# Optimization experiments

Hardware: AMD Instinct MI355X
Metric: run time of the kernel (lower is better)

Reference implementation:

```python
import jax, jax.numpy as jnp
import numpy as np

INPUT_CH = 32
INPUT_CH_VIEWS = 16
HIDDEN = 64
GEO_FEAT = 15
N_PTS = 2097152


def _kaiming(key, in_dim, out_dim):
    # mimic nn.Linear default init (kaiming uniform, fan_in)
    bound = 1.0 / np.sqrt(in_dim)
    return jax.random.uniform(key, (in_dim, out_dim), jnp.float32, -bound, bound)


def setup_inputs() -> dict:
    key = jax.random.key(0)
    ks = jax.random.split(key, 8)
    x = jax.random.normal(ks[0], (N_PTS, INPUT_CH + INPUT_CH_VIEWS), jnp.float32)
    # sigma net: 32 -> 64 -> 64 -> 16 (1 sigma + 15 geo feat), bias-free
    s0 = _kaiming(ks[1], INPUT_CH, HIDDEN)
    s1 = _kaiming(ks[2], HIDDEN, HIDDEN)
    s2 = _kaiming(ks[3], HIDDEN, 1 + GEO_FEAT)
    # color net: (16 views + 15 geo) = 31 -> 64 -> 64 -> 3, bias-free
    c0 = _kaiming(ks[4], INPUT_CH_VIEWS + GEO_FEAT, HIDDEN)
    c1 = _kaiming(ks[5], HIDDEN, HIDDEN)
    c2 = _kaiming(ks[6], HIDDEN, HIDDEN)
    c3 = _kaiming(ks[7], HIDDEN, 3)
    return {"x": x, "s0": s0, "s1": s1, "s2": s2,
            "c0": c0, "c1": c1, "c2": c2, "c3": c3}


def reference(x, s0, s1, s2, c0, c1, c2, c3):
    input_pts = x[..., :INPUT_CH]
    input_views = x[..., INPUT_CH:]
    # sigma net: ReLU between layers, no activation on last
    h = jax.nn.relu(input_pts @ s0)
    h = jax.nn.relu(h @ s1)
    h = h @ s2                      # [N, 1 + geo_feat]
    sigma = h[..., 0]
    geo_feat = h[..., 1:]
    # color net
    h = jnp.concatenate([input_views, geo_feat], axis=-1)
    h = jax.nn.relu(h @ c0)
    h = jax.nn.relu(h @ c1)
    h = jax.nn.relu(h @ c2)
    color = h @ c3                  # [N, 3]
    return jnp.concatenate([color, sigma[..., None]], axis=-1)  # [N, 4]
```

## Files before the change

### kernel.cpp

```cpp
#include <hip/hip_runtime.h>


typedef _Float16 half8  __attribute__((ext_vector_type(8)));
typedef _Float16 half4v __attribute__((ext_vector_type(4)));
typedef float    floatx4 __attribute__((ext_vector_type(4)));

#define NPTS   2097152
#define NTILES (NPTS / 64)
#define XS     72

__device__ __forceinline__ half8 load_bfrag(const float* __restrict__ W,
                                            int Kr, int Nr, int n, int kbase) {
    half8 f;
#pragma unroll
    for (int j = 0; j < 8; ++j) {
        int k = kbase + j;
        float v = (k < Kr && n < Nr) ? W[k * Nr + n] : 0.0f;
        f[j] = (_Float16)v;
    }
    return f;
}

__global__ __launch_bounds__(256, 2)
void nerf_fused(const float* __restrict__ x,
                const float* __restrict__ ws0, const float* __restrict__ ws1,
                const float* __restrict__ ws2, const float* __restrict__ wc0,
                const float* __restrict__ wc1, const float* __restrict__ wc2,
                const float* __restrict__ wc3, float* __restrict__ out) {
    __shared__ __align__(16) _Float16 sX[4][16][XS];
    __shared__ __align__(16) _Float16 sH[4][16][XS];
    __shared__ __align__(16) float    sO[4][16][4];

    const int tid  = threadIdx.x;
    const int w    = tid >> 6;
    const int lane = tid & 63;
    const int l16  = lane & 15;
    const int quad = lane >> 4;

    half8 Bs0[4], Bc0[4], Bs2[2], Bc3[2];
    half8 Bs1[4][2], Bc1[4][2], Bc2[4][2];
#pragma unroll
    for (int nt = 0; nt < 4; ++nt) {
        Bs0[nt] = load_bfrag(ws0, 32, 64, nt*16 + l16, quad*8);
        Bc0[nt] = load_bfrag(wc0, 31, 64, nt*16 + l16, quad*8);
#pragma unroll
        for (int ks = 0; ks < 2; ++ks) {
            Bs1[nt][ks] = load_bfrag(ws1, 64, 64, nt*16 + l16, ks*32 + quad*8);
            Bc1[nt][ks] = load_bfrag(wc1, 64, 64, nt*16 + l16, ks*32 + quad*8);
            Bc2[nt][ks] = load_bfrag(wc2, 64, 64, nt*16 + l16, ks*32 + quad*8);
        }
    }
#pragma unroll
    for (int ks = 0; ks < 2; ++ks) {
        Bs2[ks] = load_bfrag(ws2, 64, 16, l16, ks*32 + quad*8);
        Bc3[ks] = load_bfrag(wc3, 64,  3, l16, ks*32 + quad*8);
    }

    if (lane < 16) sX[w][lane][63] = (_Float16)0.0f;

    const floatx4 vzero = {0.f, 0.f, 0.f, 0.f};

    int srow[3], scol[3];
#pragma unroll
    for (int p = 0; p < 3; ++p) {
        int t = lane + 64*p;
        srow[p] = t / 12;
        scol[p] = (t % 12) * 4;
    }

    int tile = blockIdx.x;
    float4 xv0, xv1, xv2;
    {
        const float4* xb = (const float4*)(x + (size_t)(tile*64 + w*16) * 48);
        xv0 = xb[lane]; xv1 = xb[lane + 64]; xv2 = xb[lane + 128];
    }

    while (tile < NTILES) {
        int next = tile + gridDim.x;
        int pf = next < NTILES ? next : tile;
        const float4* xb = (const float4*)(x + (size_t)(pf*64 + w*16) * 48);
        float4 nv0 = xb[lane], nv1 = xb[lane + 64], nv2 = xb[lane + 128];

        float4 vv[3] = {xv0, xv1, xv2};
#pragma unroll
        for (int p = 0; p < 3; ++p) {
            half4v h;
            h[0] = (_Float16)vv[p].x; h[1] = (_Float16)vv[p].y;
            h[2] = (_Float16)vv[p].z; h[3] = (_Float16)vv[p].w;
            *(half4v*)&sX[w][srow[p]][scol[p]] = h;
        }

        floatx4 acc[4];

        half8 a0 = *(const half8*)&sX[w][l16][quad*8];
#pragma unroll
        for (int nt = 0; nt < 4; ++nt)
            acc[nt] = __builtin_amdgcn_mfma_f32_16x16x32_f16(a0, Bs0[nt], vzero, 0, 0, 0);
#pragma unroll
        for (int nt = 0; nt < 4; ++nt)
#pragma unroll
            for (int i = 0; i < 4; ++i)
                sH[w][quad*4 + i][nt*16 + l16] = (_Float16)fmaxf(acc[nt][i], 0.f);

        half8 a1 = *(const half8*)&sH[w][l16][quad*8];
        half8 a2 = *(const half8*)&sH[w][l16][32 + quad*8];
#pragma unroll
        for (int nt = 0; nt < 4; ++nt) {
            acc[nt] = __builtin_amdgcn_mfma_f32_16x16x32_f16(a1, Bs1[nt][0], vzero,  0, 0, 0);
            acc[nt] = __builtin_amdgcn_mfma_f32_16x16x32_f16(a2, Bs1[nt][1], acc[nt], 0, 0, 0);
        }
#pragma unroll
        for (int nt = 0; nt < 4; ++nt)
#pragma unroll
            for (int i = 0; i < 4; ++i)
                sH[w][quad*4 + i][nt*16 + l16] = (_Float16)fmaxf(acc[nt][i], 0.f);

        a1 = *(const half8*)&sH[w][l16][quad*8];
        a2 = *(const half8*)&sH[w][l16][32 + quad*8];
        floatx4 accS = __builtin_amdgcn_mfma_f32_16x16x32_f16(a1, Bs2[0], vzero, 0, 0, 0);
        accS         = __builtin_amdgcn_mfma_f32_16x16x32_f16(a2, Bs2[1], accS,  0, 0, 0);
#pragma unroll
        for (int i = 0; i < 4; ++i) {
            int row = quad*4 + i;
            if (l16 == 0) sO[w][row][3] = accS[i];
            else          sX[w][row][47 + l16] = (_Float16)accS[i];
        }

        half8 a3 = *(const half8*)&sX[w][l16][32 + quad*8];
#pragma unroll
        for (int nt = 0; nt < 4; ++nt)
            acc[nt] = __builtin_amdgcn_mfma_f32_16x16x32_f16(a3, Bc0[nt], vzero, 0, 0, 0);
#pragma unroll
        for (int nt = 0; nt < 4; ++nt)
#pragma unroll
            for (int i = 0; i < 4; ++i)
                sH[w][quad*4 + i][nt*16 + l16] = (_Float16)fmaxf(acc[nt][i], 0.f);

        a1 = *(const half8*)&sH[w][l16][quad*8];
        a2 = *(const half8*)&sH[w][l16][32 + quad*8];
#pragma unroll
        for (int nt = 0; nt < 4; ++nt) {
            acc[nt] = __builtin_amdgcn_mfma_f32_16x16x32_f16(a1, Bc1[nt][0], vzero,  0, 0, 0);
            acc[nt] = __builtin_amdgcn_mfma_f32_16x16x32_f16(a2, Bc1[nt][1], acc[nt], 0, 0, 0);
        }
#pragma unroll
        for (int nt = 0; nt < 4; ++nt)
#pragma unroll
            for (int i = 0; i < 4; ++i)
                sH[w][quad*4 + i][nt*16 + l16] = (_Float16)fmaxf(acc[nt][i], 0.f);

        a1 = *(const half8*)&sH[w][l16][quad*8];
        a2 = *(const half8*)&sH[w][l16][32 + quad*8];
#pragma unroll
        for (int nt = 0; nt < 4; ++nt) {
            acc[nt] = __builtin_amdgcn_mfma_f32_16x16x32_f16(a1, Bc2[nt][0], vzero,  0, 0, 0);
            acc[nt] = __builtin_amdgcn_mfma_f32_16x16x32_f16(a2, Bc2[nt][1], acc[nt], 0, 0, 0);
        }
#pragma unroll
        for (int nt = 0; nt < 4; ++nt)
#pragma unroll
            for (int i = 0; i < 4; ++i)
                sH[w][quad*4 + i][nt*16 + l16] = (_Float16)fmaxf(acc[nt][i], 0.f);

        a1 = *(const half8*)&sH[w][l16][quad*8];
        a2 = *(const half8*)&sH[w][l16][32 + quad*8];
        floatx4 accC = __builtin_amdgcn_mfma_f32_16x16x32_f16(a1, Bc3[0], vzero, 0, 0, 0);
        accC         = __builtin_amdgcn_mfma_f32_16x16x32_f16(a2, Bc3[1], accC,  0, 0, 0);
        if (l16 < 3) {
#pragma unroll
            for (int i = 0; i < 4; ++i)
                sO[w][quad*4 + i][l16] = accC[i];
        }

        if (lane < 16) {
            float4 o = *(const float4*)&sO[w][lane][0];
            ((float4*)out)[(size_t)tile*64 + w*16 + lane] = o;
        }

        xv0 = nv0; xv1 = nv1; xv2 = nv2;
        tile = next;
    }
}

extern "C" void kernel_launch(void* const* d_in, const int* in_sizes, int n_in,
                              void* d_out, int out_size, void* d_ws, size_t ws_size,
                              hipStream_t stream) {
    nerf_fused<<<1024, 256, 0, stream>>>(
        (const float*)d_in[0], (const float*)d_in[1], (const float*)d_in[2],
        (const float*)d_in[3], (const float*)d_in[4], (const float*)d_in[5],
        (const float*)d_in[6], (const float*)d_in[7], (float*)d_out);
}
```

Baseline: 656.3 us.

## Transpose MLP to keep activations in registers and prepack fp16 weights

The per-wave MLP is reformulated as W^T·X^T, so the MFMA output layout of one layer feeds the next layer's B operand directly. This removes the shared-memory round trips between layers, and the weight K-dimension is permuted to match. A small pre-kernel packs all weights into fp16 fragment order in the workspace, so the main kernel does one coalesced load per fragment instead of scattered fp32 gathers. Input rows are loaded directly in fragment layout, and sigma and color are written straight from the accumulators. The cost is an extra kernel launch per call and a fragile index permutation that must stay consistent.

Measured after the change: 549.3 us. 1.19x faster.

```diff
diff --git a/kernel.cpp b/kernel.cpp
--- a/kernel.cpp
+++ b/kernel.cpp
@@ -2,182 +2,150 @@
 
 
 typedef _Float16 half8  __attribute__((ext_vector_type(8)));
-typedef _Float16 half4v __attribute__((ext_vector_type(4)));
 typedef float    floatx4 __attribute__((ext_vector_type(4)));
 
 #define NPTS   2097152
 #define NTILES (NPTS / 64)
-#define XS     72
 
-__device__ __forceinline__ half8 load_bfrag(const float* __restrict__ W,
-                                            int Kr, int Nr, int n, int kbase) {
-    half8 f;
+__global__ void prep_weights(const float* __restrict__ ws0, const float* __restrict__ ws1,
+                             const float* __restrict__ ws2, const float* __restrict__ wc0,
+                             const float* __restrict__ wc1, const float* __restrict__ wc2,
+                             const float* __restrict__ wc3, _Float16* __restrict__ wpack) {
+    int t = blockIdx.x * blockDim.x + threadIdx.x;
+    if (t >= 36 * 64) return;
+    int fid = t >> 6, lane = t & 63, l16 = lane & 15, q = lane >> 4;
 #pragma unroll
     for (int j = 0; j < 8; ++j) {
-        int k = kbase + j;
-        float v = (k < Kr && n < Nr) ? W[k * Nr + n] : 0.0f;
-        f[j] = (_Float16)v;
+        int phi = (2 * 0 + (j >> 2)) * 16 + q * 4 + (j & 3);
+        float v = 0.f;
+        if (fid < 4) {
+            v = ws0[(q * 8 + j) * 64 + fid * 16 + l16];
+        } else if (fid < 12) {
+            int mt = (fid - 4) >> 1, c = (fid - 4) & 1;
+            int p = (2 * c + (j >> 2)) * 16 + q * 4 + (j & 3);
+            v = ws1[p * 64 + mt * 16 + l16];
+        } else if (fid < 14) {
+            int c = fid - 12;
+            int p = (2 * c + (j >> 2)) * 16 + q * 4 + (j & 3);
+            v = ws2[p * 16 + l16];
+        } else if (fid < 18) {
+            int mt = fid - 14;
+            if (j < 4) v = wc0[(q * 4 + j) * 64 + mt * 16 + l16];
+            else {
+                int g = q * 4 + (j - 4);
+                v = (g == 0) ? 0.f : wc0[(15 + g) * 64 + mt * 16 + l16];
+            }
+        } else if (fid < 26) {
+            int mt = (fid - 18) >> 1, c = (fid - 18) & 1;
+            int p = (2 * c + (j >> 2)) * 16 + q * 4 + (j & 3);
+            v = wc1[p * 64 + mt * 16 + l16];
+        } else if (fid < 34) {
+            int mt = (fid - 26) >> 1, c = (fid - 26) & 1;
+            int p = (2 * c + (j >> 2)) * 16 + q * 4 + (j & 3);
+            v = wc2[p * 64 + mt * 16 + l16];
+        } else {
+            int c = fid - 34;
+            int p = (2 * c + (j >> 2)) * 16 + q * 4 + (j & 3);
+            v = (l16 < 3) ? wc3[p * 3 + l16] : 0.f;
+        }
+        (void)phi;
+        wpack[t * 8 + j] = (_Float16)v;
     }
-    return f;
+}
+
+__device__ __forceinline__ half8 packrelu(floatx4 a, floatx4 b) {
+    half8 r;
+    r[0] = (_Float16)fmaxf(a[0], 0.f); r[1] = (_Float16)fmaxf(a[1], 0.f);
+    r[2] = (_Float16)fmaxf(a[2], 0.f); r[3] = (_Float16)fmaxf(a[3], 0.f);
+    r[4] = (_Float16)fmaxf(b[0], 0.f); r[5] = (_Float16)fmaxf(b[1], 0.f);
+    r[6] = (_Float16)fmaxf(b[2], 0.f); r[7] = (_Float16)fmaxf(b[3], 0.f);
+    return r;
 }
 
 __global__ __launch_bounds__(256, 2)
-void nerf_fused(const float* __restrict__ x,
-                const float* __restrict__ ws0, const float* __restrict__ ws1,
-                const float* __restrict__ ws2, const float* __restrict__ wc0,
-                const float* __restrict__ wc1, const float* __restrict__ wc2,
-                const float* __restrict__ wc3, float* __restrict__ out) {
-    __shared__ __align__(16) _Float16 sX[4][16][XS];
-    __shared__ __align__(16) _Float16 sH[4][16][XS];
-    __shared__ __align__(16) float    sO[4][16][4];
+void nerf_fused(const float* __restrict__ x, const _Float16* __restrict__ wpack,
+                float* __restrict__ out) {
+    const int lane = threadIdx.x & 63;
+    const int w    = threadIdx.x >> 6;
+    const int l16  = lane & 15;
+    const int q    = lane >> 4;
 
-    const int tid  = threadIdx.x;
-    const int w    = tid >> 6;
-    const int lane = tid & 63;
-    const int l16  = lane & 15;
-    const int quad = lane >> 4;
+    half8 W[36];
+    const half8* wp = (const half8*)wpack;
+#pragma unroll
+    for (int f = 0; f < 36; ++f) W[f] = wp[f * 64 + lane];
 
-    half8 Bs0[4], Bc0[4], Bs2[2], Bc3[2];
-    half8 Bs1[4][2], Bc1[4][2], Bc2[4][2];
-#pragma unroll
-    for (int nt = 0; nt < 4; ++nt) {
-        Bs0[nt] = load_bfrag(ws0, 32, 64, nt*16 + l16, quad*8);
-        Bc0[nt] = load_bfrag(wc0, 31, 64, nt*16 + l16, quad*8);
-#pragma unroll
-        for (int ks = 0; ks < 2; ++ks) {
-            Bs1[nt][ks] = load_bfrag(ws1, 64, 64, nt*16 + l16, ks*32 + quad*8);
-            Bc1[nt][ks] = load_bfrag(wc1, 64, 64, nt*16 + l16, ks*32 + quad*8);
-            Bc2[nt][ks] = load_bfrag(wc2, 64, 64, nt*16 + l16, ks*32 + quad*8);
-        }
-    }
-#pragma unroll
-    for (int ks = 0; ks < 2; ++ks) {
-        Bs2[ks] = load_bfrag(ws2, 64, 16, l16, ks*32 + quad*8);
-        Bc3[ks] = load_bfrag(wc3, 64,  3, l16, ks*32 + quad*8);
-    }
-
-    if (lane < 16) sX[w][lane][63] = (_Float16)0.0f;
-
-    const floatx4 vzero = {0.f, 0.f, 0.f, 0.f};
-
-    int srow[3], scol[3];
-#pragma unroll
-    for (int p = 0; p < 3; ++p) {
-        int t = lane + 64*p;
-        srow[p] = t / 12;
-        scol[p] = (t % 12) * 4;
-    }
+    const floatx4 vz = {0.f, 0.f, 0.f, 0.f};
+    const float4* xb = (const float4*)x;
 
     int tile = blockIdx.x;
-    float4 xv0, xv1, xv2;
+    float4 vA, vB, vC;
     {
-        const float4* xb = (const float4*)(x + (size_t)(tile*64 + w*16) * 48);
-        xv0 = xb[lane]; xv1 = xb[lane + 64]; xv2 = xb[lane + 128];
+        size_t base = (size_t)(tile * 64 + w * 16 + l16) * 12;
+        vA = xb[base + q * 2]; vB = xb[base + q * 2 + 1]; vC = xb[base + 8 + q];
     }
 
     while (tile < NTILES) {
         int next = tile + gridDim.x;
         int pf = next < NTILES ? next : tile;
-        const float4* xb = (const float4*)(x + (size_t)(pf*64 + w*16) * 48);
-        float4 nv0 = xb[lane], nv1 = xb[lane + 64], nv2 = xb[lane + 128];
+        size_t nbase = (size_t)(pf * 64 + w * 16 + l16) * 12;
+        float4 nA = xb[nbase + q * 2], nB = xb[nbase + q * 2 + 1], nC = xb[nbase + 8 + q];
 
-        float4 vv[3] = {xv0, xv1, xv2};
+        half8 b0, b1;
+        b0[0] = (_Float16)vA.x; b0[1] = (_Float16)vA.y; b0[2] = (_Float16)vA.z; b0[3] = (_Float16)vA.w;
+        b0[4] = (_Float16)vB.x; b0[5] = (_Float16)vB.y; b0[6] = (_Float16)vB.z; b0[7] = (_Float16)vB.w;
+        floatx4 acc[4], a2[4];
 #pragma unroll
-        for (int p = 0; p < 3; ++p) {
-            half4v h;
-            h[0] = (_Float16)vv[p].x; h[1] = (_Float16)vv[p].y;
-            h[2] = (_Float16)vv[p].z; h[3] = (_Float16)vv[p].w;
-            *(half4v*)&sX[w][srow[p]][scol[p]] = h;
+        for (int mt = 0; mt < 4; ++mt)
+            acc[mt] = __builtin_amdgcn_mfma_f32_16x16x32_f16(W[mt], b0, vz, 0, 0, 0);
+
+        b0 = packrelu(acc[0], acc[1]); b1 = packrelu(acc[2], acc[3]);
+#pragma unroll
+        for (int mt = 0; mt < 4; ++mt) {
+            a2[mt] = __builtin_amdgcn_mfma_f32_16x16x32_f16(W[4 + mt * 2], b0, vz,     0, 0, 0);
+            a2[mt] = __builtin_amdgcn_mfma_f32_16x16x32_f16(W[5 + mt * 2], b1, a2[mt], 0, 0, 0);
         }
 
-        floatx4 acc[4];
+        b0 = packrelu(a2[0], a2[1]); b1 = packrelu(a2[2], a2[3]);
+        floatx4 accS;
+        accS = __builtin_amdgcn_mfma_f32_16x16x32_f16(W[12], b0, vz,   0, 0, 0);
+        accS = __builtin_amdgcn_mfma_f32_16x16x32_f16(W[13], b1, accS, 0, 0, 0);
+        float sigma = accS[0];
 
-        half8 a0 = *(const half8*)&sX[w][l16][quad*8];
+        half8 bc;
+        bc[0] = (_Float16)vC.x; bc[1] = (_Float16)vC.y; bc[2] = (_Float16)vC.z; bc[3] = (_Float16)vC.w;
+        bc[4] = (q == 0) ? (_Float16)0.f : (_Float16)accS[0];
+        bc[5] = (_Float16)accS[1]; bc[6] = (_Float16)accS[2]; bc[7] = (_Float16)accS[3];
 #pragma unroll
-        for (int nt = 0; nt < 4; ++nt)
-            acc[nt] = __builtin_amdgcn_mfma_f32_16x16x32_f16(a0, Bs0[nt], vzero, 0, 0, 0);
+        for (int mt = 0; mt < 4; ++mt)
+            acc[mt] = __builtin_amdgcn_mfma_f32_16x16x32_f16(W[14 + mt], bc, vz, 0, 0, 0);
+
+        b0 = packrelu(acc[0], acc[1]); b1 = packrelu(acc[2], acc[3]);
 #pragma unroll
-        for (int nt = 0; nt < 4; ++nt)
-#pragma unroll
-            for (int i = 0; i < 4; ++i)
-                sH[w][quad*4 + i][nt*16 + l16] = (_Float16)fmaxf(acc[nt][i], 0.f);
-
-        half8 a1 = *(const half8*)&sH[w][l16][quad*8];
-        half8 a2 = *(const half8*)&sH[w][l16][32 + quad*8];
-#pragma unroll
-        for (int nt = 0; nt < 4; ++nt) {
-            acc[nt] = __builtin_amdgcn_mfma_f32_16x16x32_f16(a1, Bs1[nt][0], vzero,  0, 0, 0);
-            acc[nt] = __builtin_amdgcn_mfma_f32_16x16x32_f16(a2, Bs1[nt][1], acc[nt], 0, 0, 0);
-        }
-#pragma unroll
-        for (int nt = 0; nt < 4; ++nt)
-#pragma unroll
-            for (int i = 0; i < 4; ++i)
-                sH[w][quad*4 + i][nt*16 + l16] = (_Float16)fmaxf(acc[nt][i], 0.f);
-
-        a1 = *(const half8*)&sH[w][l16][quad*8];
-        a2 = *(const half8*)&sH[w][l16][32 + quad*8];
-        floatx4 accS = __builtin_amdgcn_mfma_f32_16x16x32_f16(a1, Bs2[0], vzero, 0, 0, 0);
-        accS         = __builtin_amdgcn_mfma_f32_16x16x32_f16(a2, Bs2[1], accS,  0, 0, 0);
-#pragma unroll
-        for (int i = 0; i < 4; ++i) {
-            int row = quad*4 + i;
-            if (l16 == 0) sO[w][row][3] = accS[i];
-            else          sX[w][row][47 + l16] = (_Float16)accS[i];
+        for (int mt = 0; mt < 4; ++mt) {
+            a2[mt] = __builtin_amdgcn_mfma_f32_16x16x32_f16(W[18 + mt * 2], b0, vz,     0, 0, 0);
+            a2[mt] = __builtin_amdgcn_mfma_f32_16x16x32_f16(W[19 + mt * 2], b1, a2[mt], 0, 0, 0);
         }
 
-        half8 a3 = *(const half8*)&sX[w][l16][32 + quad*8];
+        b0 = packrelu(a2[0], a2[1]); b1 = packrelu(a2[2], a2[3]);
 #pragma unroll
-        for (int nt = 0; nt < 4; ++nt)
-            acc[nt] = __builtin_amdgcn_mfma_f32_16x16x32_f16(a3, Bc0[nt], vzero, 0, 0, 0);
-#pragma unroll
-        for (int nt = 0; nt < 4; ++nt)
-#pragma unroll
-            for (int i = 0; i < 4; ++i)
-                sH[w][quad*4 + i][nt*16 + l16] = (_Float16)fmaxf(acc[nt][i], 0.f);
-
-        a1 = *(const half8*)&sH[w][l16][quad*8];
-        a2 = *(const half8*)&sH[w][l16][32 + quad*8];
-#pragma unroll
-        for (int nt = 0; nt < 4; ++nt) {
-            acc[nt] = __builtin_amdgcn_mfma_f32_16x16x32_f16(a1, Bc1[nt][0], vzero,  0, 0, 0);
-            acc[nt] = __builtin_amdgcn_mfma_f32_16x16x32_f16(a2, Bc1[nt][1], acc[nt], 0, 0, 0);
-        }
-#pragma unroll
-        for (int nt = 0; nt < 4; ++nt)
-#pragma unroll
-            for (int i = 0; i < 4; ++i)
-                sH[w][quad*4 + i][nt*16 + l16] = (_Float16)fmaxf(acc[nt][i], 0.f);
-
-        a1 = *(const half8*)&sH[w][l16][quad*8];
-        a2 = *(const half8*)&sH[w][l16][32 + quad*8];
-#pragma unroll
-        for (int nt = 0; nt < 4; ++nt) {
-            acc[nt] = __builtin_amdgcn_mfma_f32_16x16x32_f16(a1, Bc2[nt][0], vzero,  0, 0, 0);
-            acc[nt] = __builtin_amdgcn_mfma_f32_16x16x32_f16(a2, Bc2[nt][1], acc[nt], 0, 0, 0);
-        }
-#pragma unroll
-        for (int nt = 0; nt < 4; ++nt)
-#pragma unroll
-            for (int i = 0; i < 4; ++i)
-                sH[w][quad*4 + i][nt*16 + l16] = (_Float16)fmaxf(acc[nt][i], 0.f);
-
-        a1 = *(const half8*)&sH[w][l16][quad*8];
-        a2 = *(const half8*)&sH[w][l16][32 + quad*8];
-        floatx4 accC = __builtin_amdgcn_mfma_f32_16x16x32_f16(a1, Bc3[0], vzero, 0, 0, 0);
-        accC         = __builtin_amdgcn_mfma_f32_16x16x32_f16(a2, Bc3[1], accC,  0, 0, 0);
-        if (l16 < 3) {
-#pragma unroll
-            for (int i = 0; i < 4; ++i)
-                sO[w][quad*4 + i][l16] = accC[i];
+        for (int mt = 0; mt < 4; ++mt) {
+            acc[mt] = __builtin_amdgcn_mfma_f32_16x16x32_f16(W[26 + mt * 2], b0, vz,      0, 0, 0);
+            acc[mt] = __builtin_amdgcn_mfma_f32_16x16x32_f16(W[27 + mt * 2], b1, acc[mt], 0, 0, 0);
         }
 
+        b0 = packrelu(acc[0], acc[1]); b1 = packrelu(acc[2], acc[3]);
+        floatx4 accC;
+        accC = __builtin_amdgcn_mfma_f32_16x16x32_f16(W[34], b0, vz,   0, 0, 0);
+        accC = __builtin_amdgcn_mfma_f32_16x16x32_f16(W[35], b1, accC, 0, 0, 0);
+
         if (lane < 16) {
-            float4 o = *(const float4*)&sO[w][lane][0];
-            ((float4*)out)[(size_t)tile*64 + w*16 + lane] = o;
+            float4 o;
+            o.x = accC[0]; o.y = accC[1]; o.z = accC[2]; o.w = sigma;
+            ((float4*)out)[(size_t)tile * 64 + w * 16 + lane] = o;
         }
 
-        xv0 = nv0; xv1 = nv1; xv2 = nv2;
+        vA = nA; vB = nB; vC = nC;
         tile = next;
     }
 }
@@ -185,8 +153,10 @@
 extern "C" void kernel_launch(void* const* d_in, const int* in_sizes, int n_in,
                               void* d_out, int out_size, void* d_ws, size_t ws_size,
                               hipStream_t stream) {
-    nerf_fused<<<1024, 256, 0, stream>>>(
-        (const float*)d_in[0], (const float*)d_in[1], (const float*)d_in[2],
-        (const float*)d_in[3], (const float*)d_in[4], (const float*)d_in[5],
-        (const float*)d_in[6], (const float*)d_in[7], (float*)d_out);
+    _Float16* wpack = (_Float16*)d_ws;
+    prep_weights<<<9, 256, 0, stream>>>(
+        (const float*)d_in[1], (const float*)d_in[2], (const float*)d_in[3],
+        (const float*)d_in[4], (const float*)d_in[5], (const float*)d_in[6],
+        (const float*)d_in[7], wpack);
+    nerf_fused<<<1024, 256, 0, stream>>>((const float*)d_in[0], wpack, (float*)d_out);
 }
```
